# Kernel tuning notes

Hardware: AMD Instinct MI355X
Metric: run time of the kernel (lower is better)

The kernel has to match this reference:

```python
import jax, jax.numpy as jnp
import numpy as np
from jax import lax

TAU = 0.5       # opt.tau
EPSILON = 1e-3  # opt.epsilon


def setup_inputs() -> dict:
    key = jax.random.key(0)
    k1, k2, k3, k4 = jax.random.split(key, 4)
    B, Cin, H, W = 32, 64, 64, 64
    Cout, KS = 256, 5
    x = jax.random.normal(k1, (B, Cin, H, W), dtype=jnp.float32)
    # W_ff: OIHW conv kernel (Kaiming-ish scale)
    W_ff = jax.random.normal(k2, (Cout, Cin, KS, KS), dtype=jnp.float32) * (1.0 / np.sqrt(Cin * KS * KS))
    # W_rec: 1x1 recurrent conv, stored as [out, out]; small so the LCA loop converges
    W_rec = jax.random.normal(k3, (Cout, Cout), dtype=jnp.float32) * 0.01
    threshold = 0.1 * jax.random.normal(k4, (Cout,), dtype=jnp.float32)
    return {"x": x, "W_ff": W_ff, "W_rec": W_rec, "threshold": threshold, "max_n_iter": 20}


def _fro(v):
    return jnp.linalg.norm(v.ravel())


def _forward(x, W_ff, W_rec, threshold, max_n_iter):
    max_iter = max_n_iter * int(1.0 / TAU)
    # u_0 = W_ff * input  (valid conv, no bias)  -> [B, Cout, Ho, Wo]
    u0 = lax.conv_general_dilated(x, W_ff, window_strides=(1, 1), padding='VALID',
                                  dimension_numbers=('NCHW', 'OIHW', 'NCHW'))
    thr = threshold[None, :, None, None]
    a0 = jax.nn.relu(u0 - thr)
    u_init = jnp.zeros_like(u0)

    def cond(state):
        _, _, i, converged = state
        return jnp.logical_and(jnp.logical_not(converged), i <= max_iter)

    def body(state):
        u, a, i, _ = state
        # 1x1 recurrent conv == channel matmul
        rec = jnp.einsum('oi,bixy->boxy', W_rec, a)
        u_new = (1.0 - TAU) * u + TAU * (u0 - rec)
        a_new = jax.nn.relu(u_new - thr)
        converged = (_fro(u_new - u) / _fro(u_new)) < EPSILON
        return (u_new, a_new, i + 1, converged)

    _, a_final, _, _ = lax.while_loop(cond, body, (u_init, a0, jnp.int32(0), jnp.array(False)))
    # original torch code detaches activities throughout the loop and at return
    return lax.stop_gradient(a_final)


def reference(x, W_ff, W_rec, threshold, max_n_iter):
    return _forward(x, W_ff, W_rec, threshold, max_n_iter)
```

## Files before the change

kernel.cpp:

```cpp
#include <hip/hip_runtime.h>


typedef __attribute__((ext_vector_type(8))) short short8;
typedef __attribute__((ext_vector_type(4))) float f32x4;

#define NTOT 115200
#define CHW  262144
#define HW2  4096
#define LDA  264
#define LDC  42

__device__ __forceinline__ unsigned short f2bf(float f) {
  unsigned int u = __float_as_uint(f);
  unsigned int r = u + 0x7FFFu + ((u >> 16) & 1u);
  return (unsigned short)(r >> 16);
}
__device__ __forceinline__ float bf2f(unsigned short h) {
  return __uint_as_float(((unsigned int)h) << 16);
}
__device__ __forceinline__ unsigned short f2h(float f) {
  _Float16 x = (_Float16)f;
  unsigned short r;
  __builtin_memcpy(&r, &x, 2);
  return r;
}
__device__ __forceinline__ float h2f(unsigned short h) {
  _Float16 x;
  __builtin_memcpy(&x, &h, 2);
  return (float)x;
}

__global__ void cast_weights(const float* __restrict__ wff_f,
                             const float* __restrict__ wrec_f,
                             unsigned short* __restrict__ wff,
                             unsigned short* __restrict__ wrec_sw) {
  int tid = blockIdx.x * 256 + threadIdx.x;
  if (tid < 409600) {
    int o = tid / 1600, k = tid % 1600;
    int kk = k >> 6, ci = k & 63;
    wff[tid] = f2bf(wff_f[o * 1600 + ci * 25 + kk]);
  } else if (tid < 409600 + 65536) {
    int i = tid - 409600;
    int o = i >> 8, ic = i & 255;
    wrec_sw[(((ic >> 3) << 8) + o) * 8 + (ic & 7)] = f2bf(wrec_f[i]);
  }
}

__global__ __launch_bounds__(256) void transpose_x(
    const float* __restrict__ x, unsigned short* __restrict__ xt) {
  int g = blockIdx.x * 256 + threadIdx.x;
  const float* src = x + (long)(g >> 12) * CHW + (g & 4095);
  unsigned short* dst = xt + (long)g * 64;
#pragma unroll
  for (int oct = 0; oct < 8; ++oct) {
    alignas(16) unsigned short tmp[8];
#pragma unroll
    for (int d = 0; d < 8; ++d)
      tmp[d] = f2bf(src[(oct * 8 + d) * HW2]);
    *(int4*)(dst + oct * 8) = *(const int4*)tmp;
  }
}

__global__ __launch_bounds__(256) void conv_kernel(
    const unsigned short* __restrict__ xt,
    const unsigned short* __restrict__ wff,
    unsigned short* __restrict__ u0_nc) {
  __shared__ short As[128 * LDC];
  __shared__ short Bs[128 * LDC];
  const int t = threadIdx.x;
  const int n0 = blockIdx.x * 128;
  const int oc0 = blockIdx.y * 128;
  const int lane = t & 63, w = t >> 6;
  const int q = lane >> 4, r = lane & 15;
  const int woc = w >> 1, wn = w & 1;
  const int qt = t & 3, mrow = t >> 2;

  int xbase[2];
#pragma unroll
  for (int p = 0; p < 2; ++p) {
    int n = n0 + p * 64 + mrow;
    int bb = n / 3600, rem = n - bb * 3600;
    int yy = rem / 60, xx = rem - yy * 60;
    xbase[p] = (bb * 4096 + yy * 64 + xx) * 64 + qt * 8;
  }

  f32x4 acc[4][4];
#pragma unroll
  for (int i = 0; i < 4; i++)
#pragma unroll
    for (int j = 0; j < 4; j++) acc[i][j] = (f32x4){0.f, 0.f, 0.f, 0.f};

  for (int c = 0; c < 50; ++c) {
    const int k0 = c * 32;
    const int kk = c >> 1;
    const int ky = kk / 5, kx = kk - ky * 5;
    const int choff = (ky * 64 + kx) * 64 + (c & 1) * 32;

    __syncthreads();
#pragma unroll
    for (int p = 0; p < 2; ++p) {
      int m = p * 64 + mrow;
      *(int4*)(&Bs[m * LDC + qt * 8]) =
          *(const int4*)(wff + (oc0 + m) * 1600 + k0 + qt * 8);
    }
#pragma unroll
    for (int p = 0; p < 2; ++p) {
      int m = p * 64 + mrow;
      *(int4*)(&As[m * LDC + qt * 8]) = *(const int4*)(xt + xbase[p] + choff);
    }
    __syncthreads();

    short8 xf[4], wf[4];
#pragma unroll
    for (int j = 0; j < 4; j++)
      xf[j] = *(const short8*)(&As[(wn * 64 + j * 16 + r) * LDC + q * 8]);
#pragma unroll
    for (int i = 0; i < 4; i++)
      wf[i] = *(const short8*)(&Bs[(woc * 64 + i * 16 + r) * LDC + q * 8]);
#pragma unroll
    for (int i = 0; i < 4; i++)
#pragma unroll
      for (int j = 0; j < 4; j++)
        acc[i][j] = __builtin_amdgcn_mfma_f32_16x16x32_bf16(wf[i], xf[j],
                                                            acc[i][j], 0, 0, 0);
  }

#pragma unroll
  for (int j = 0; j < 4; j++) {
    const int n = n0 + wn * 64 + j * 16 + r;
#pragma unroll
    for (int i = 0; i < 4; i++) {
      const int oc = oc0 + woc * 64 + i * 16 + q * 4;
      alignas(8) unsigned short up[4];
#pragma unroll
      for (int d = 0; d < 4; ++d) up[d] = f2h(acc[i][j][d]);
      *(uint2*)(&u0_nc[n * 256 + oc]) = *(const uint2*)up;
    }
  }
}

__device__ __forceinline__ void gemm_rec8(short* a_lds,
                                          const unsigned short* __restrict__
                                              wrec_sw,
                                          int w, int q, int r) {
  f32x4 acc[2][4];
#pragma unroll
  for (int i = 0; i < 2; i++)
#pragma unroll
    for (int j = 0; j < 4; j++) acc[i][j] = (f32x4){0.f, 0.f, 0.f, 0.f};

#pragma unroll
  for (int c = 0; c < 8; ++c) {
    short8 afr[2], bfr[4];
#pragma unroll
    for (int i = 0; i < 2; i++)
      afr[i] = *(const short8*)(wrec_sw +
               (((c * 4 + q) << 8) + w * 32 + i * 16 + r) * 8);
#pragma unroll
    for (int j = 0; j < 4; j++)
      bfr[j] = *(const short8*)(&a_lds[(j * 16 + r) * LDA + c * 32 + q * 8]);
#pragma unroll
    for (int i = 0; i < 2; i++)
#pragma unroll
      for (int j = 0; j < 4; j++)
        acc[i][j] = __builtin_amdgcn_mfma_f32_16x16x32_bf16(afr[i], bfr[j],
                                                            acc[i][j], 0, 0, 0);
  }
  __syncthreads();
#pragma unroll
  for (int j = 0; j < 4; j++) {
    const int nr = j * 16 + r;
#pragma unroll
    for (int i = 0; i < 2; i++) {
      const int oc = w * 32 + i * 16 + q * 4;
      alignas(8) unsigned short rp[4];
#pragma unroll
      for (int d = 0; d < 4; ++d) rp[d] = f2h(acc[i][j][d]);
      *(uint2*)(&a_lds[nr * LDA + oc]) = *(const uint2*)rp;
    }
  }
  __syncthreads();
}

template <int FIRST>
__global__ __launch_bounds__(512, 4) void iter_pair(
    const unsigned short* __restrict__ wrec_sw,
    const unsigned short* __restrict__ u0, const float* __restrict__ thr,
    const unsigned short* __restrict__ uin,
    unsigned short* __restrict__ uA, unsigned short* __restrict__ uB,
    float* __restrict__ norms, int* __restrict__ flag, int itA) {
  __shared__ short a_lds[64 * LDA];
  __shared__ float red[32];

  const int t = threadIdx.x;
  if (!FIRST) {
    if (*(volatile int*)flag) return;
    float dA = 0.f, nA = 0.f, dB = 0.f, nB = 0.f;
#pragma unroll
    for (int s = 0; s < 8; ++s) {
      dA += norms[(itA - 2) * 16 + s];
      nA += norms[(itA - 2) * 16 + 8 + s];
      dB += norms[(itA - 1) * 16 + s];
      nB += norms[(itA - 1) * 16 + 8 + s];
    }
    if (dA < 1e-6f * nA || dB < 1e-6f * nB) {
      if (t == 0) *flag = 1;
      return;
    }
  }

  const int n0 = blockIdx.x * 64;
  const int ch = t & 31;
  const int row0 = t >> 5;
  const int occh = ch * 8;
  const int lane = t & 63, w = t >> 6;
  const int q = lane >> 4, r = lane & 15;

  float4 th0 = *(const float4*)(thr + occh);
  float4 th1 = *(const float4*)(thr + occh + 4);
  float thc[8] = {th0.x, th0.y, th0.z, th0.w, th1.x, th1.y, th1.z, th1.w};

  int4 sv[4];
  int4 u0c[4];

#pragma unroll
  for (int p = 0; p < 4; ++p) {
    const int base = (n0 + row0 + p * 16) * 256 + occh;
    u0c[p] = *(const int4*)(u0 + base);
    if (FIRST)
      sv[p] = u0c[p];
    else
      sv[p] = *(const int4*)(uin + base);
    const unsigned short* hs = (const unsigned short*)&sv[p];
    alignas(16) unsigned short ap[8];
#pragma unroll
    for (int d = 0; d < 8; ++d) {
      float a = h2f(hs[d]) - thc[d];
      ap[d] = f2bf(a > 0.f ? a : 0.f);
    }
    *(int4*)(&a_lds[(row0 + p * 16) * LDA + occh]) = *(const int4*)ap;
  }
  __syncthreads();

  gemm_rec8(a_lds, wrec_sw, w, q, r);

  float d2A = 0.f, n2A = 0.f;
#pragma unroll
  for (int p = 0; p < 4; ++p) {
    const int base = (n0 + row0 + p * 16) * 256 + occh;
    int4 rr = *(const int4*)(&a_lds[(row0 + p * 16) * LDA + occh]);
    const unsigned short* rs = (const unsigned short*)&rr;
    const unsigned short* us = (const unsigned short*)&u0c[p];
    const unsigned short* hs = (const unsigned short*)&sv[p];
    alignas(16) unsigned short up[8];
    alignas(16) unsigned short ap[8];
#pragma unroll
    for (int d = 0; d < 8; ++d) {
      float uo = FIRST ? 0.f : h2f(hs[d]);
      float un = 0.5f * uo + 0.5f * (h2f(us[d]) - h2f(rs[d]));
      float df = un - uo;
      d2A += df * df;
      n2A += un * un;
      up[d] = f2h(un);
      float ur = h2f(up[d]);
      float a = ur - thc[d];
      ap[d] = f2bf(a > 0.f ? a : 0.f);
    }
    sv[p] = *(const int4*)up;
    *(int4*)(uA + base) = sv[p];
    *(int4*)(&a_lds[(row0 + p * 16) * LDA + occh]) = *(const int4*)ap;
  }
  __syncthreads();

  gemm_rec8(a_lds, wrec_sw, w, q, r);

  float d2B = 0.f, n2B = 0.f;
#pragma unroll
  for (int p = 0; p < 4; ++p) {
    const int base = (n0 + row0 + p * 16) * 256 + occh;
    int4 rr = *(const int4*)(&a_lds[(row0 + p * 16) * LDA + occh]);
    const unsigned short* rs = (const unsigned short*)&rr;
    const unsigned short* us = (const unsigned short*)&u0c[p];
    const unsigned short* hs = (const unsigned short*)&sv[p];
    alignas(16) unsigned short up[8];
#pragma unroll
    for (int d = 0; d < 8; ++d) {
      float uo = h2f(hs[d]);
      float un = 0.5f * uo + 0.5f * (h2f(us[d]) - h2f(rs[d]));
      float df = un - uo;
      d2B += df * df;
      n2B += un * un;
      up[d] = f2h(un);
    }
    *(int4*)(uB + base) = *(const int4*)up;
  }

#pragma unroll
  for (int off = 32; off; off >>= 1) {
    d2A += __shfl_down(d2A, off, 64);
    n2A += __shfl_down(n2A, off, 64);
    d2B += __shfl_down(d2B, off, 64);
    n2B += __shfl_down(n2B, off, 64);
  }
  if (lane == 0) {
    red[w] = d2A; red[8 + w] = n2A; red[16 + w] = d2B; red[24 + w] = n2B;
  }
  __syncthreads();
  if (t == 0) {
    float a0 = 0.f, a1 = 0.f, a2 = 0.f, a3 = 0.f;
#pragma unroll
    for (int s = 0; s < 8; ++s) {
      a0 += red[s]; a1 += red[8 + s]; a2 += red[16 + s]; a3 += red[24 + s];
    }
    const int slot = blockIdx.x & 7;
    atomicAdd(&norms[itA * 16 + slot], a0);
    atomicAdd(&norms[itA * 16 + 8 + slot], a1);
    atomicAdd(&norms[(itA + 1) * 16 + slot], a2);
    atomicAdd(&norms[(itA + 1) * 16 + 8 + slot], a3);
  }
}

template <int FIRST>
__global__ __launch_bounds__(512, 4) void iter_one(
    const unsigned short* __restrict__ wrec_sw,
    const unsigned short* __restrict__ u0, const float* __restrict__ thr,
    const unsigned short* __restrict__ uin, unsigned short* __restrict__ uout,
    float* __restrict__ norms, int* __restrict__ flag, int it) {
  __shared__ short a_lds[64 * LDA];
  __shared__ float red[16];

  const int t = threadIdx.x;
  if (!FIRST) {
    if (*(volatile int*)flag) return;
    float dA = 0.f, nA = 0.f, dB = 0.f, nB = 0.f;
#pragma unroll
    for (int s = 0; s < 8; ++s) {
      dA += norms[(it - 2) * 16 + s];
      nA += norms[(it - 2) * 16 + 8 + s];
      dB += norms[(it - 1) * 16 + s];
      nB += norms[(it - 1) * 16 + 8 + s];
    }
    if (dA < 1e-6f * nA || dB < 1e-6f * nB) {
      if (t == 0) *flag = 1;
      return;
    }
  }

  const int n0 = blockIdx.x * 64;
  const int ch = t & 31;
  const int row0 = t >> 5;
  const int occh = ch * 8;
  const int lane = t & 63, w = t >> 6;
  const int q = lane >> 4, r = lane & 15;

  float4 th0 = *(const float4*)(thr + occh);
  float4 th1 = *(const float4*)(thr + occh + 4);
  float thc[8] = {th0.x, th0.y, th0.z, th0.w, th1.x, th1.y, th1.z, th1.w};

  int4 sv[4];
  int4 u0c[4];
#pragma unroll
  for (int p = 0; p < 4; ++p) {
    const int base = (n0 + row0 + p * 16) * 256 + occh;
    u0c[p] = *(const int4*)(u0 + base);
    if (FIRST)
      sv[p] = u0c[p];
    else
      sv[p] = *(const int4*)(uin + base);
    const unsigned short* hs = (const unsigned short*)&sv[p];
    alignas(16) unsigned short ap[8];
#pragma unroll
    for (int d = 0; d < 8; ++d) {
      float a = h2f(hs[d]) - thc[d];
      ap[d] = f2bf(a > 0.f ? a : 0.f);
    }
    *(int4*)(&a_lds[(row0 + p * 16) * LDA + occh]) = *(const int4*)ap;
  }
  __syncthreads();

  gemm_rec8(a_lds, wrec_sw, w, q, r);

  float d2 = 0.f, n2 = 0.f;
#pragma unroll
  for (int p = 0; p < 4; ++p) {
    const int base = (n0 + row0 + p * 16) * 256 + occh;
    int4 rr = *(const int4*)(&a_lds[(row0 + p * 16) * LDA + occh]);
    const unsigned short* rs = (const unsigned short*)&rr;
    const unsigned short* us = (const unsigned short*)&u0c[p];
    const unsigned short* hs = (const unsigned short*)&sv[p];
    alignas(16) unsigned short up[8];
#pragma unroll
    for (int d = 0; d < 8; ++d) {
      float uo = FIRST ? 0.f : h2f(hs[d]);
      float un = 0.5f * uo + 0.5f * (h2f(us[d]) - h2f(rs[d]));
      float df = un - uo;
      d2 += df * df;
      n2 += un * un;
      up[d] = f2h(un);
    }
    *(int4*)(uout + base) = *(const int4*)up;
  }

#pragma unroll
  for (int off = 32; off; off >>= 1) {
    d2 += __shfl_down(d2, off, 64);
    n2 += __shfl_down(n2, off, 64);
  }
  if (lane == 0) { red[w] = d2; red[8 + w] = n2; }
  __syncthreads();
  if (t == 0) {
    float a0 = 0.f, a1 = 0.f;
#pragma unroll
    for (int s = 0; s < 8; ++s) { a0 += red[s]; a1 += red[8 + s]; }
    const int slot = blockIdx.x & 7;
    atomicAdd(&norms[it * 16 + slot], a0);
    atomicAdd(&norms[it * 16 + 8 + slot], a1);
  }
}

__global__ void sel_kernel(const float* __restrict__ norms,
                           int* __restrict__ sel) {
  int it = 1;
  for (; it <= 41; ++it) {
    float d = 0.f, n = 0.f;
    for (int s = 0; s < 8; ++s) {
      d += norms[it * 16 + s];
      n += norms[it * 16 + 8 + s];
    }
    if (d < 1e-6f * n) break;
  }
  if (it > 41) it = 41;
  *sel = (it & 1) ? 0 : 1;
}
__global__ void set_sel(int* __restrict__ sel, int v) { *sel = v; }

__global__ __launch_bounds__(256) void final_out(
    const unsigned short* __restrict__ uA,
    const unsigned short* __restrict__ uB, const int* __restrict__ sel,
    const float* __restrict__ thr, float* __restrict__ out) {
  const unsigned short* u = (*sel) ? uB : uA;
  const int t = threadIdx.x, lane = t & 63, w = t >> 6;
  const int n = blockIdx.x * 64 + lane;
  const int b = n / 3600, s = n - b * 3600;
  float* ob = out + (long)b * 921600 + s;
  const unsigned short* ub = u + (long)n * 256 + w * 64;
#pragma unroll
  for (int g = 0; g < 8; ++g) {
    int4 raw = *(const int4*)(ub + g * 8);
    const unsigned short* rs = (const unsigned short*)&raw;
#pragma unroll
    for (int d = 0; d < 8; ++d) {
      int oc = w * 64 + g * 8 + d;
      float v = h2f(rs[d]) - thr[oc];
      ob[oc * 3600] = v > 0.f ? v : 0.f;
    }
  }
}

extern "C" void kernel_launch(void* const* d_in, const int* in_sizes, int n_in,
                              void* d_out, int out_size, void* d_ws,
                              size_t ws_size, hipStream_t stream) {
  const float* x      = (const float*)d_in[0];
  const float* wff_f  = (const float*)d_in[1];
  const float* wrec_f = (const float*)d_in[2];
  const float* thr    = (const float*)d_in[3];
  float* out = (float*)d_out;

  char* ws = (char*)d_ws;
  int* flag = (int*)ws;
  int* sel  = (int*)(ws + 8);
  float* norms = (float*)(ws + 64);
  unsigned short* wff     = (unsigned short*)(ws + 4096);
  unsigned short* wrec_sw = (unsigned short*)(ws + 823296);
  unsigned short* xt = (unsigned short*)(ws + 983040);
  unsigned short* uB = (unsigned short*)(ws + 983040);
  unsigned short* u0 = (unsigned short*)(ws + 59965440);
  unsigned short* uA = (unsigned short*)(ws + 118947840);
  const size_t NEEDED = 118947840ULL + 58982400ULL;

  hipMemsetAsync(d_ws, 0, 4096, stream);
  cast_weights<<<1856, 256, 0, stream>>>(wff_f, wrec_f, wff, wrec_sw);
  transpose_x<<<512, 256, 0, stream>>>(x, xt);
  conv_kernel<<<dim3(900, 2), 256, 0, stream>>>(xt, wff, u0);

  if (ws_size >= NEEDED) {
    iter_pair<1><<<1800, 512, 0, stream>>>(wrec_sw, u0, thr, uB, uA, uB,
                                           norms, flag, 1);
    for (int itA = 3; itA <= 39; itA += 2)
      iter_pair<0><<<1800, 512, 0, stream>>>(wrec_sw, u0, thr, uB, uA, uB,
                                             norms, flag, itA);
    iter_one<0><<<1800, 512, 0, stream>>>(wrec_sw, u0, thr, uB, uA, norms,
                                          flag, 41);
    sel_kernel<<<1, 1, 0, stream>>>(norms, sel);
  } else {
    iter_one<1><<<1800, 512, 0, stream>>>(wrec_sw, u0, thr, uB, uB, norms,
                                          flag, 1);
    for (int it = 2; it <= 41; ++it)
      iter_one<0><<<1800, 512, 0, stream>>>(wrec_sw, u0, thr, uB, uB, norms,
                                            flag, it);
    set_sel<<<1, 1, 0, stream>>>(sel, 1);
  }
  final_out<<<1800, 256, 0, stream>>>(uA, uB, sel, thr, out);
}
```

Baseline: 1.212 ms.

## Keep recurrent GEMM results in registers by remapping elementwise work to MFMA layout

```diff
diff --git a/kernel.cpp b/kernel.cpp
--- a/kernel.cpp
+++ b/kernel.cpp
@@ -8,7 +8,7 @@
 #define CHW  262144
 #define HW2  4096
 #define LDA  264
-#define LDC  42
+#define LDC  40
 
 __device__ __forceinline__ unsigned short f2bf(float f) {
   unsigned int u = __float_as_uint(f);
@@ -139,11 +139,11 @@
   }
 }
 
-__device__ __forceinline__ void gemm_rec8(short* a_lds,
+__device__ __forceinline__ void gemm_acc8(const short* a_lds,
                                           const unsigned short* __restrict__
                                               wrec_sw,
-                                          int w, int q, int r) {
-  f32x4 acc[2][4];
+                                          int w, int q, int r,
+                                          f32x4 acc[2][4]) {
 #pragma unroll
   for (int i = 0; i < 2; i++)
 #pragma unroll
@@ -166,20 +166,6 @@
         acc[i][j] = __builtin_amdgcn_mfma_f32_16x16x32_bf16(afr[i], bfr[j],
                                                             acc[i][j], 0, 0, 0);
   }
-  __syncthreads();
-#pragma unroll
-  for (int j = 0; j < 4; j++) {
-    const int nr = j * 16 + r;
-#pragma unroll
-    for (int i = 0; i < 2; i++) {
-      const int oc = w * 32 + i * 16 + q * 4;
-      alignas(8) unsigned short rp[4];
-#pragma unroll
-      for (int d = 0; d < 4; ++d) rp[d] = f2h(acc[i][j][d]);
-      *(uint2*)(&a_lds[nr * LDA + oc]) = *(const uint2*)rp;
-    }
-  }
-  __syncthreads();
 }
 
 template <int FIRST>
@@ -210,90 +196,105 @@
   }
 
   const int n0 = blockIdx.x * 64;
-  const int ch = t & 31;
-  const int row0 = t >> 5;
-  const int occh = ch * 8;
   const int lane = t & 63, w = t >> 6;
   const int q = lane >> 4, r = lane & 15;
-
-  float4 th0 = *(const float4*)(thr + occh);
-  float4 th1 = *(const float4*)(thr + occh + 4);
-  float thc[8] = {th0.x, th0.y, th0.z, th0.w, th1.x, th1.y, th1.z, th1.w};
-
-  int4 sv[4];
-  int4 u0c[4];
-
-#pragma unroll
-  for (int p = 0; p < 4; ++p) {
-    const int base = (n0 + row0 + p * 16) * 256 + occh;
-    u0c[p] = *(const int4*)(u0 + base);
-    if (FIRST)
-      sv[p] = u0c[p];
-    else
-      sv[p] = *(const int4*)(uin + base);
-    const unsigned short* hs = (const unsigned short*)&sv[p];
-    alignas(16) unsigned short ap[8];
-#pragma unroll
-    for (int d = 0; d < 8; ++d) {
-      float a = h2f(hs[d]) - thc[d];
-      ap[d] = f2bf(a > 0.f ? a : 0.f);
-    }
-    *(int4*)(&a_lds[(row0 + p * 16) * LDA + occh]) = *(const int4*)ap;
-  }
+  const int ob = (n0 + r) * 256 + w * 32 + q * 4;
+
+  float thc[2][4];
+#pragma unroll
+  for (int i = 0; i < 2; ++i) {
+    float4 th = *(const float4*)(thr + w * 32 + i * 16 + q * 4);
+    thc[i][0] = th.x; thc[i][1] = th.y; thc[i][2] = th.z; thc[i][3] = th.w;
+  }
+
+  uint2 sv[2][4], u0c[2][4];
+#pragma unroll
+  for (int j = 0; j < 4; ++j)
+#pragma unroll
+    for (int i = 0; i < 2; ++i) {
+      const int off = ob + j * 4096 + i * 16;
+      u0c[i][j] = *(const uint2*)(u0 + off);
+      sv[i][j] = FIRST ? u0c[i][j] : *(const uint2*)(uin + off);
+    }
+
+#pragma unroll
+  for (int j = 0; j < 4; ++j)
+#pragma unroll
+    for (int i = 0; i < 2; ++i) {
+      const unsigned short* hs = (const unsigned short*)&sv[i][j];
+      alignas(8) unsigned short ap[4];
+#pragma unroll
+      for (int d = 0; d < 4; ++d) {
+        float a = h2f(hs[d]) - thc[i][d];
+        ap[d] = f2bf(a > 0.f ? a : 0.f);
+      }
+      *(uint2*)(&a_lds[(j * 16 + r) * LDA + w * 32 + i * 16 + q * 4]) =
+          *(const uint2*)ap;
+    }
   __syncthreads();
 
-  gemm_rec8(a_lds, wrec_sw, w, q, r);
+  f32x4 acc[2][4];
+  gemm_acc8(a_lds, wrec_sw, w, q, r, acc);
 
   float d2A = 0.f, n2A = 0.f;
 #pragma unroll
-  for (int p = 0; p < 4; ++p) {
-    const int base = (n0 + row0 + p * 16) * 256 + occh;
-    int4 rr = *(const int4*)(&a_lds[(row0 + p * 16) * LDA + occh]);
-    const unsigned short* rs = (const unsigned short*)&rr;
-    const unsigned short* us = (const unsigned short*)&u0c[p];
-    const unsigned short* hs = (const unsigned short*)&sv[p];
-    alignas(16) unsigned short up[8];
-    alignas(16) unsigned short ap[8];
-#pragma unroll
-    for (int d = 0; d < 8; ++d) {
-      float uo = FIRST ? 0.f : h2f(hs[d]);
-      float un = 0.5f * uo + 0.5f * (h2f(us[d]) - h2f(rs[d]));
-      float df = un - uo;
-      d2A += df * df;
-      n2A += un * un;
-      up[d] = f2h(un);
-      float ur = h2f(up[d]);
-      float a = ur - thc[d];
-      ap[d] = f2bf(a > 0.f ? a : 0.f);
-    }
-    sv[p] = *(const int4*)up;
-    *(int4*)(uA + base) = sv[p];
-    *(int4*)(&a_lds[(row0 + p * 16) * LDA + occh]) = *(const int4*)ap;
-  }
+  for (int j = 0; j < 4; ++j)
+#pragma unroll
+    for (int i = 0; i < 2; ++i) {
+      const unsigned short* us = (const unsigned short*)&u0c[i][j];
+      const unsigned short* hs = (const unsigned short*)&sv[i][j];
+      alignas(8) unsigned short up[4];
+#pragma unroll
+      for (int d = 0; d < 4; ++d) {
+        float uo = FIRST ? 0.f : h2f(hs[d]);
+        float un = 0.5f * uo + 0.5f * (h2f(us[d]) - acc[i][j][d]);
+        float df = un - uo;
+        d2A += df * df;
+        n2A += un * un;
+        up[d] = f2h(un);
+      }
+      sv[i][j] = *(const uint2*)up;
+      *(uint2*)(uA + ob + j * 4096 + i * 16) = sv[i][j];
+    }
   __syncthreads();
 
-  gemm_rec8(a_lds, wrec_sw, w, q, r);
+#pragma unroll
+  for (int j = 0; j < 4; ++j)
+#pragma unroll
+    for (int i = 0; i < 2; ++i) {
+      const unsigned short* hs = (const unsigned short*)&sv[i][j];
+      alignas(8) unsigned short ap[4];
+#pragma unroll
+      for (int d = 0; d < 4; ++d) {
+        float a = h2f(hs[d]) - thc[i][d];
+        ap[d] = f2bf(a > 0.f ? a : 0.f);
+      }
+      *(uint2*)(&a_lds[(j * 16 + r) * LDA + w * 32 + i * 16 + q * 4]) =
+          *(const uint2*)ap;
+    }
+  __syncthreads();
+
+  gemm_acc8(a_lds, wrec_sw, w, q, r, acc);
 
   float d2B = 0.f, n2B = 0.f;
 #pragma unroll
-  for (int p = 0; p < 4; ++p) {
-    const int base = (n0 + row0 + p * 16) * 256 + occh;
-    int4 rr = *(const int4*)(&a_lds[(row0 + p * 16) * LDA + occh]);
-    const unsigned short* rs = (const unsigned short*)&rr;
-    const unsigned short* us = (const unsigned short*)&u0c[p];
-    const unsigned short* hs = (const unsigned short*)&sv[p];
-    alignas(16) unsigned short up[8];
-#pragma unroll
-    for (int d = 0; d < 8; ++d) {
-      float uo = h2f(hs[d]);
-      float un = 0.5f * uo + 0.5f * (h2f(us[d]) - h2f(rs[d]));
-      float df = un - uo;
-      d2B += df * df;
-      n2B += un * un;
-      up[d] = f2h(un);
-    }
-    *(int4*)(uB + base) = *(const int4*)up;
-  }
+  for (int j = 0; j < 4; ++j)
+#pragma unroll
+    for (int i = 0; i < 2; ++i) {
+      const unsigned short* us = (const unsigned short*)&u0c[i][j];
+      const unsigned short* hs = (const unsigned short*)&sv[i][j];
+      alignas(8) unsigned short up[4];
+#pragma unroll
+      for (int d = 0; d < 4; ++d) {
+        float uo = h2f(hs[d]);
+        float un = 0.5f * uo + 0.5f * (h2f(us[d]) - acc[i][j][d]);
+        float df = un - uo;
+        d2B += df * df;
+        n2B += un * un;
+        up[d] = f2h(un);
+      }
+      *(uint2*)(uB + ob + j * 4096 + i * 16) = *(const uint2*)up;
+    }
 
 #pragma unroll
   for (int off = 32; off; off >>= 1) {
@@ -347,59 +348,65 @@
   }
 
   const int n0 = blockIdx.x * 64;
-  const int ch = t & 31;
-  const int row0 = t >> 5;
-  const int occh = ch * 8;
   const int lane = t & 63, w = t >> 6;
   const int q = lane >> 4, r = lane & 15;
-
-  float4 th0 = *(const float4*)(thr + occh);
-  float4 th1 = *(const float4*)(thr + occh + 4);
-  float thc[8] = {th0.x, th0.y, th0.z, th0.w, th1.x, th1.y, th1.z, th1.w};
-
-  int4 sv[4];
-  int4 u0c[4];
-#pragma unroll
-  for (int p = 0; p < 4; ++p) {
-    const int base = (n0 + row0 + p * 16) * 256 + occh;
-    u0c[p] = *(const int4*)(u0 + base);
-    if (FIRST)
-      sv[p] = u0c[p];
-    else
-      sv[p] = *(const int4*)(uin + base);
-    const unsigned short* hs = (const unsigned short*)&sv[p];
-    alignas(16) unsigned short ap[8];
-#pragma unroll
-    for (int d = 0; d < 8; ++d) {
-      float a = h2f(hs[d]) - thc[d];
-      ap[d] = f2bf(a > 0.f ? a : 0.f);
-    }
-    *(int4*)(&a_lds[(row0 + p * 16) * LDA + occh]) = *(const int4*)ap;
-  }
+  const int ob = (n0 + r) * 256 + w * 32 + q * 4;
+
+  float thc[2][4];
+#pragma unroll
+  for (int i = 0; i < 2; ++i) {
+    float4 th = *(const float4*)(thr + w * 32 + i * 16 + q * 4);
+    thc[i][0] = th.x; thc[i][1] = th.y; thc[i][2] = th.z; thc[i][3] = th.w;
+  }
+
+  uint2 sv[2][4], u0c[2][4];
+#pragma unroll
+  for (int j = 0; j < 4; ++j)
+#pragma unroll
+    for (int i = 0; i < 2; ++i) {
+      const int off = ob + j * 4096 + i * 16;
+      u0c[i][j] = *(const uint2*)(u0 + off);
+      sv[i][j] = FIRST ? u0c[i][j] : *(const uint2*)(uin + off);
+    }
+
+#pragma unroll
+  for (int j = 0; j < 4; ++j)
+#pragma unroll
+    for (int i = 0; i < 2; ++i) {
+      const unsigned short* hs = (const unsigned short*)&sv[i][j];
+      alignas(8) unsigned short ap[4];
+#pragma unroll
+      for (int d = 0; d < 4; ++d) {
+        float a = h2f(hs[d]) - thc[i][d];
+        ap[d] = f2bf(a > 0.f ? a : 0.f);
+      }
+      *(uint2*)(&a_lds[(j * 16 + r) * LDA + w * 32 + i * 16 + q * 4]) =
+          *(const uint2*)ap;
+    }
   __syncthreads();
 
-  gemm_rec8(a_lds, wrec_sw, w, q, r);
+  f32x4 acc[2][4];
+  gemm_acc8(a_lds, wrec_sw, w, q, r, acc);
 
   float d2 = 0.f, n2 = 0.f;
 #pragma unroll
-  for (int p = 0; p < 4; ++p) {
-    const int base = (n0 + row0 + p * 16) * 256 + occh;
-    int4 rr = *(const int4*)(&a_lds[(row0 + p * 16) * LDA + occh]);
-    const unsigned short* rs = (const unsigned short*)&rr;
-    const unsigned short* us = (const unsigned short*)&u0c[p];
-    const unsigned short* hs = (const unsigned short*)&sv[p];
-    alignas(16) unsigned short up[8];
-#pragma unroll
-    for (int d = 0; d < 8; ++d) {
-      float uo = FIRST ? 0.f : h2f(hs[d]);
-      float un = 0.5f * uo + 0.5f * (h2f(us[d]) - h2f(rs[d]));
-      float df = un - uo;
-      d2 += df * df;
-      n2 += un * un;
-      up[d] = f2h(un);
-    }
-    *(int4*)(uout + base) = *(const int4*)up;
-  }
+  for (int j = 0; j < 4; ++j)
+#pragma unroll
+    for (int i = 0; i < 2; ++i) {
+      const unsigned short* us = (const unsigned short*)&u0c[i][j];
+      const unsigned short* hs = (const unsigned short*)&sv[i][j];
+      alignas(8) unsigned short up[4];
+#pragma unroll
+      for (int d = 0; d < 4; ++d) {
+        float uo = FIRST ? 0.f : h2f(hs[d]);
+        float un = 0.5f * uo + 0.5f * (h2f(us[d]) - acc[i][j][d]);
+        float df = un - uo;
+        d2 += df * df;
+        n2 += un * un;
+        up[d] = f2h(un);
+      }
+      *(uint2*)(uout + ob + j * 4096 + i * 16) = *(const uint2*)up;
+    }
 
 #pragma unroll
   for (int off = 32; off; off >>= 1) {
```

New measurement: 1.311 ms. 8.2% more time.
